# Kernel tuning notes

Hardware: AMD Instinct MI355X
Metric: run time of the kernel (lower is better)

Reference implementation:

```python
import jax, jax.numpy as jnp
import numpy as np

N = 100000
E = 3200000
IN_C, H1, H2 = 512, 64, 32


def gcn_norm(edge_index, edge_weight, num_nodes):
    """PyG gcn_norm with add_self_loops=True: D^-1/2 (A+I) D^-1/2 edge weights."""
    row, col = edge_index[0], edge_index[1]
    loop = jnp.arange(num_nodes, dtype=edge_index.dtype)
    row = jnp.concatenate([row, loop])
    col = jnp.concatenate([col, loop])
    w = jnp.concatenate([edge_weight, jnp.ones((num_nodes,), edge_weight.dtype)])
    deg = jax.ops.segment_sum(w, col, num_segments=num_nodes)
    dinv = jnp.where(deg > 0, jax.lax.rsqrt(jnp.maximum(deg, 1e-12)), 0.0)
    wnorm = dinv[row] * w * dinv[col]
    return row, col, wnorm


def gcn_conv(x, W, b, row, col, wnorm, num_nodes):
    h = x @ W                                   # [N, out] linear first (out <= in)
    msg = wnorm[:, None] * h[row]               # gather + per-edge scale  [E+N, out]
    out = jax.ops.segment_sum(msg, col, num_segments=num_nodes)
    return out + b


def setup_inputs() -> dict:
    key = jax.random.key(0)
    ks = jax.random.split(key, 9)
    x = jax.random.normal(ks[0], (N, IN_C), dtype=jnp.float32)
    edge_index = jax.random.randint(ks[1], (2, E), 0, N, dtype=jnp.int64)
    edge_weight = jax.random.uniform(ks[2], (E,), dtype=jnp.float32)
    # Glorot-style init for GCN linear weights, zero bias (PyG defaults).
    def glorot(k, fan_in, fan_out):
        s = np.sqrt(6.0 / (fan_in + fan_out)).astype(np.float32)
        return jax.random.uniform(k, (fan_in, fan_out), jnp.float32, -s, s)
    return {
        "x": x,
        "edge_index": edge_index,
        "edge_weight": edge_weight,
        "W1": glorot(ks[3], IN_C, H1), "b1": jnp.zeros((H1,), jnp.float32),
        "W2": glorot(ks[4], H1, H2),  "b2": jnp.zeros((H2,), jnp.float32),
        "W3": glorot(ks[5], H2, 1),   "b3": jnp.zeros((1,), jnp.float32),
    }


def reference(x, edge_index, edge_weight, W1, b1, W2, b2, W3, b3):
    # Inference mode: dropout is identity (training=False).
    row, col, wnorm = gcn_norm(edge_index, edge_weight, N)  # cached=True: shared across layers
    h = jax.nn.relu(gcn_conv(x, W1, b1, row, col, wnorm, N))
    h = jax.nn.relu(gcn_conv(h, W2, b2, row, col, wnorm, N))
    h = gcn_conv(h, W3, b3, row, col, wnorm, N)
    return h.reshape(-1)  # [N]
```

## Files before the change

kernel.cpp:

```cpp
#include <hip/hip_runtime.h>

constexpr int BLK = 256;
constexpr int NBLKBIN = 512;
constexpr int MAXNB   = 1024;

typedef __bf16 bf16x8 __attribute__((ext_vector_type(8)));
typedef float  f32x4  __attribute__((ext_vector_type(4)));

__device__ __forceinline__ float blo(unsigned u) { return __uint_as_float(u << 16); }
__device__ __forceinline__ float bhi(unsigned u) { return __uint_as_float(u & 0xffff0000u); }

__device__ __forceinline__ int detect64(const void* ei) {
    const int* p = (const int*)ei;
    int is64 = 1;
#pragma unroll
    for (int i = 0; i < 16; ++i)
        if (p[2 * i + 1] != 0) is64 = 0;
    return is64;
}

__device__ __forceinline__ int load_idx(const void* ei, size_t pos, int is64) {
    if (is64) return (int)((const long long*)ei)[pos];
    return ((const int*)ei)[pos];
}

__global__ void k_prep(const float* __restrict__ W1, const float* __restrict__ W2,
                       __bf16* __restrict__ Wtf, __bf16* __restrict__ Wtf2,
                       int* __restrict__ bkt_cnt, int nb) {
    const int b = blockIdx.x;
    const int t = threadIdx.x;
    if (b < 16) {
        int i = b * 256 + t;
        int lane = i & 63;
        int tt   = (i >> 6) & 3;
        int k0c  = i >> 8;
        int col  = tt * 16 + (lane & 15);
        int kbase = k0c * 32 + (lane >> 4) * 8;
        bf16x8 v;
#pragma unroll
        for (int j = 0; j < 8; ++j) v[j] = (__bf16)W1[(size_t)(kbase + j) * 64 + col];
        *(bf16x8*)(Wtf + (size_t)i * 8) = v;
    } else if (b == 16) {
        int i = t;
        int lane = i & 63;
        int ct   = i >> 6;
        int tt = ct & 1, chunk = ct >> 1;
        int col  = tt * 16 + (lane & 15);
        int kbase = chunk * 32 + (lane >> 4) * 8;
        bf16x8 v;
#pragma unroll
        for (int j = 0; j < 8; ++j) v[j] = (__bf16)W2[(size_t)(kbase + j) * 32 + col];
        *(bf16x8*)(Wtf2 + (size_t)i * 8) = v;
    } else {
        for (int i = t; i < nb; i += 256) bkt_cnt[i] = 0;
    }
}

__global__ __launch_bounds__(256) void k_fat(const void* __restrict__ ei, int e,
                                             int* __restrict__ bucket_cnt,
                                             int* __restrict__ blkbase, int nb,
                                             const float* __restrict__ X,
                                             const __bf16* __restrict__ Wtf,
                                             __bf16* __restrict__ H, int nrows) {
    __shared__ int hist[MAXNB];
    const int t = threadIdx.x;
    if (blockIdx.x < NBLKBIN) {
        for (int b = t; b < nb; b += 256) hist[b] = 0;
        __syncthreads();
        const int is64 = detect64(ei);
        const int chunk = (e + NBLKBIN - 1) / NBLKBIN;
        const int i0 = blockIdx.x * chunk;
        const int i1 = min(e, i0 + chunk);
        for (int i = i0 + t; i < i1; i += 256) {
            int dst = load_idx(ei, (size_t)e + i, is64);
            atomicAdd(&hist[dst >> 7], 1);
        }
        __syncthreads();
        int* myb = blkbase + (size_t)blockIdx.x * MAXNB;
        for (int b = t; b < nb; b += 256) {
            int c = hist[b];
            int base = 0;
            if (c) base = atomicAdd(&bucket_cnt[b], c);
            myb[b] = base;
        }
        return;
    }
    const int bid  = blockIdx.x - NBLKBIN;
    const int wave = t >> 6;
    const int lane = t & 63;
    const int l15  = lane & 15;
    const int lq   = lane >> 4;
    const long rbase = (long)bid * 256 + wave * 64;

    const float4* xr[4];
#pragma unroll
    for (int rg = 0; rg < 4; ++rg) {
        long ar = rbase + rg * 16 + l15;
        if (ar >= nrows) ar = nrows - 1;
        xr[rg] = (const float4*)(X + (size_t)ar * 512) + lq * 2;
    }

    f32x4 acc[4][4];
#pragma unroll
    for (int rg = 0; rg < 4; ++rg)
#pragma unroll
        for (int tt = 0; tt < 4; ++tt) acc[rg][tt] = f32x4{0.f, 0.f, 0.f, 0.f};

    float4 pa[2][4][2];
#pragma unroll
    for (int s = 0; s < 2; ++s)
#pragma unroll
        for (int rg = 0; rg < 4; ++rg) {
            pa[s][rg][0] = xr[rg][s * 8];
            pa[s][rg][1] = xr[rg][s * 8 + 1];
        }

#pragma unroll
    for (int k0c = 0; k0c < 16; ++k0c) {
        const int s = k0c & 1;
        bf16x8 af[4];
#pragma unroll
        for (int rg = 0; rg < 4; ++rg) {
            float4 a0 = pa[s][rg][0], a1 = pa[s][rg][1];
            af[rg][0] = (__bf16)a0.x; af[rg][1] = (__bf16)a0.y;
            af[rg][2] = (__bf16)a0.z; af[rg][3] = (__bf16)a0.w;
            af[rg][4] = (__bf16)a1.x; af[rg][5] = (__bf16)a1.y;
            af[rg][6] = (__bf16)a1.z; af[rg][7] = (__bf16)a1.w;
        }
        if (k0c + 2 < 16) {
#pragma unroll
            for (int rg = 0; rg < 4; ++rg) {
                pa[s][rg][0] = xr[rg][(k0c + 2) * 8];
                pa[s][rg][1] = xr[rg][(k0c + 2) * 8 + 1];
            }
        }
#pragma unroll
        for (int tt = 0; tt < 4; ++tt) {
            bf16x8 bf_ = *(const bf16x8*)(Wtf + ((size_t)(k0c * 4 + tt) * 64 + lane) * 8);
#pragma unroll
            for (int rg = 0; rg < 4; ++rg)
                acc[rg][tt] = __builtin_amdgcn_mfma_f32_16x16x32_bf16(af[rg], bf_, acc[rg][tt], 0, 0, 0);
        }
    }
#pragma unroll
    for (int rg = 0; rg < 4; ++rg)
#pragma unroll
    for (int tt = 0; tt < 4; ++tt)
#pragma unroll
    for (int r = 0; r < 4; ++r) {
        long row = rbase + rg * 16 + lq * 4 + r;
        if (row < nrows) H[(size_t)row * 64 + tt * 16 + l15] = (__bf16)acc[rg][tt][r];
    }
}

__global__ __launch_bounds__(256) void k_binscatter(const void* __restrict__ ei,
                                                    const float* __restrict__ ew, int e,
                                                    const int* __restrict__ bkt_cnt,
                                                    const int* __restrict__ blkbase,
                                                    int2* __restrict__ binned, int nb) {
    __shared__ int scn[256];
    __shared__ int hist[MAXNB];
    const int t = threadIdx.x;
    const int base = t * 4;
    int v[4]; int s = 0;
#pragma unroll
    for (int k = 0; k < 4; ++k) {
        int i = base + k;
        v[k] = (i < nb) ? bkt_cnt[i] : 0;
        s += v[k];
    }
    scn[t] = s;
    __syncthreads();
    for (int d = 1; d < 256; d <<= 1) {
        int x = (t >= d) ? scn[t - d] : 0;
        __syncthreads();
        scn[t] += x;
        __syncthreads();
    }
    int excl = (t == 0) ? 0 : scn[t - 1];
    const int* myb = blkbase + (size_t)blockIdx.x * MAXNB;
#pragma unroll
    for (int k = 0; k < 4; ++k) {
        int i = base + k;
        if (i < nb) hist[i] = excl + myb[i];
        excl += v[k];
    }
    __syncthreads();
    const int is64 = detect64(ei);
    const int chunk = (e + NBLKBIN - 1) / NBLKBIN;
    const int i0 = blockIdx.x * chunk;
    const int i1 = min(e, i0 + chunk);
    for (int i = i0 + t; i < i1; i += 256) {
        int dst = load_idx(ei, (size_t)e + i, is64);
        int src = load_idx(ei, (size_t)i, is64);
        float w = ew[i];
        int bin = dst >> 7;
        int pos = atomicAdd(&hist[bin], 1);
        binned[pos] = make_int2(src | ((dst & 127) << 20), __float_as_int(w));
    }
}

__device__ __forceinline__ void bucket_prefix(const int* __restrict__ bkt_cnt, int nb,
                                              int* scn, int* pfx) {
    const int t = threadIdx.x;
    const int base = t * 4;
    int v[4]; int s = 0;
#pragma unroll
    for (int k = 0; k < 4; ++k) {
        int i = base + k;
        v[k] = (i < nb) ? bkt_cnt[i] : 0;
        s += v[k];
    }
    scn[t] = s;
    __syncthreads();
    for (int d = 1; d < 256; d <<= 1) {
        int x = (t >= d) ? scn[t - d] : 0;
        __syncthreads();
        scn[t] += x;
        __syncthreads();
    }
    int run = (t == 0) ? 0 : scn[t - 1];
#pragma unroll
    for (int k = 0; k < 4; ++k) {
        run += v[k];
        pfx[base + k] = run;
    }
    __syncthreads();
}

__global__ __launch_bounds__(256) void k_degoffs(const int* __restrict__ bkt_cnt,
                                                 const int2* __restrict__ binned,
                                                 float* __restrict__ dinv,
                                                 int* __restrict__ offs, int n, int e, int nb) {
    __shared__ int                scn[256];
    __shared__ int                pfx[MAXNB];
    __shared__ int                icnt[128];
    __shared__ unsigned long long facc[128];
    __shared__ int                scn2[128];
    const int t = threadIdx.x;
    const int b = blockIdx.x;
    bucket_prefix(bkt_cnt, nb, scn, pfx);
    const int j0 = (b == 0) ? 0 : pfx[b - 1];
    const int j1 = pfx[b];
    if (t < 128) { icnt[t] = 0; facc[t] = 0ull; }
    __syncthreads();
    const float SCALE = 1099511627776.f;
    for (int j = j0 + t; j < j1; j += 256) {
        int2 p = binned[j];
        int dl = ((unsigned)p.x) >> 20;
        atomicAdd(&icnt[dl], 1);
        atomicAdd(&facc[dl], (unsigned long long)(__int_as_float(p.y) * SCALE));
    }
    __syncthreads();
    if (t < 128) {
        int nd = b * 128 + t;
        if (nd < n) dinv[nd] = rsqrtf(fmaf((float)facc[t], 1.f / 1099511627776.f, 1.0f));
        scn2[t] = icnt[t];
    }
    __syncthreads();
    for (int d = 1; d < 128; d <<= 1) {
        int x = 0;
        if (t < 128 && t >= d) x = scn2[t - d];
        __syncthreads();
        if (t < 128) scn2[t] += x;
        __syncthreads();
    }
    if (t < 128) {
        int excl = (t == 0) ? 0 : scn2[t - 1];
        int nd = b * 128 + t;
        if (nd < n) offs[nd] = j0 + excl;
    }
    if (b == 0 && t == 0) offs[n] = e;
}

__global__ __launch_bounds__(256) void k_place(const int* __restrict__ bkt_cnt,
                                               const int2* __restrict__ binned,
                                               const int* __restrict__ offs,
                                               const float* __restrict__ dinv,
                                               int2* __restrict__ csrp, int n, int nb) {
    __shared__ int   scn[256];
    __shared__ int   pfx[MAXNB];
    __shared__ int   cur[128];
    __shared__ float ddst[128];
    const int t = threadIdx.x;
    const int b = blockIdx.x;
    bucket_prefix(bkt_cnt, nb, scn, pfx);
    const int j0 = (b == 0) ? 0 : pfx[b - 1];
    const int j1 = pfx[b];
    if (t < 128) {
        int nd = b * 128 + t;
        cur[t]  = (nd < n) ? offs[nd] : 0;
        ddst[t] = (nd < n) ? dinv[nd] : 0.f;
    }
    __syncthreads();
    for (int j = j0 + t; j < j1; j += 256) {
        int2 p = binned[j];
        int dl  = ((unsigned)p.x) >> 20;
        int src = p.x & 0xFFFFF;
        int pos = atomicAdd(&cur[dl], 1);
        float w2 = __int_as_float(p.y) * dinv[src] * ddst[dl];
        csrp[pos] = make_int2(src, __float_as_int(w2));
    }
}

__global__ __launch_bounds__(256) void k_gemm2_mfma(const __bf16* __restrict__ A,
                                                    const __bf16* __restrict__ Wtf2,
                                                    __bf16* __restrict__ H, int nrows) {
    const int wave = threadIdx.x >> 6;
    const int lane = threadIdx.x & 63;
    const int l15  = lane & 15;
    const int lq   = lane >> 4;
    const long rbase = (long)blockIdx.x * 64 + wave * 16;

    long arow = rbase + l15;
    if (arow >= nrows) arow = nrows - 1;

    f32x4 acc[2] = {{0.f,0.f,0.f,0.f},{0.f,0.f,0.f,0.f}};
#pragma unroll
    for (int c = 0; c < 2; ++c) {
        bf16x8 af = *(const bf16x8*)(A + (size_t)arow * 64 + c * 32 + lq * 8);
#pragma unroll
        for (int t = 0; t < 2; ++t) {
            bf16x8 bf_ = *(const bf16x8*)(Wtf2 + ((size_t)(c * 2 + t) * 64 + lane) * 8);
            acc[t] = __builtin_amdgcn_mfma_f32_16x16x32_bf16(af, bf_, acc[t], 0, 0, 0);
        }
    }
#pragma unroll
    for (int t = 0; t < 2; ++t)
#pragma unroll
    for (int r = 0; r < 4; ++r) {
        long row = rbase + lq * 4 + r;
        if (row < nrows) H[(size_t)row * 32 + t * 16 + l15] = (__bf16)acc[t][r];
    }
}

template <int K, int EPI>
__global__ __launch_bounds__(256) void k_prop_bf(const int* __restrict__ offs,
                                                 const int2* __restrict__ csrp,
                                                 const __bf16* __restrict__ hb,
                                                 const float* __restrict__ dinv,
                                                 const float* __restrict__ bias,
                                                 const float* __restrict__ W3,
                                                 void* __restrict__ outv, int n) {
    constexpr int SUB = K / 4;
    constexpr int NPW = 64 / SUB;
    constexpr int NPB = 4 * NPW;
    const int t    = threadIdx.x;
    const int lane = t & 63;
    const int wave = t >> 6;
    const int chq  = lane & (SUB - 1);
    const int sub  = lane / SUB;
    const long nd  = (long)blockIdx.x * NPB + wave * NPW + sub;
    if (nd >= n) return;

    const unsigned short* h = (const unsigned short*)hb;
    const int j0 = offs[nd], j1 = offs[nd + 1];
    float a0 = 0.f, a1 = 0.f, a2 = 0.f, a3 = 0.f;
    int j = j0;
    for (; j + 3 < j1; j += 4) {
        int2 p0 = csrp[j];
        int2 p1 = csrp[j + 1];
        int2 p2 = csrp[j + 2];
        int2 p3 = csrp[j + 3];
        uint2 u0 = *(const uint2*)(h + (size_t)p0.x * K + 4 * chq);
        uint2 u1 = *(const uint2*)(h + (size_t)p1.x * K + 4 * chq);
        uint2 u2 = *(const uint2*)(h + (size_t)p2.x * K + 4 * chq);
        uint2 u3 = *(const uint2*)(h + (size_t)p3.x * K + 4 * chq);
        float w0 = __int_as_float(p0.y), w1 = __int_as_float(p1.y);
        float w2 = __int_as_float(p2.y), w3 = __int_as_float(p3.y);
        a0 = fmaf(w0, blo(u0.x), a0); a1 = fmaf(w0, bhi(u0.x), a1);
        a2 = fmaf(w0, blo(u0.y), a2); a3 = fmaf(w0, bhi(u0.y), a3);
        a0 = fmaf(w1, blo(u1.x), a0); a1 = fmaf(w1, bhi(u1.x), a1);
        a2 = fmaf(w1, blo(u1.y), a2); a3 = fmaf(w1, bhi(u1.y), a3);
        a0 = fmaf(w2, blo(u2.x), a0); a1 = fmaf(w2, bhi(u2.x), a1);
        a2 = fmaf(w2, blo(u2.y), a2); a3 = fmaf(w2, bhi(u2.y), a3);
        a0 = fmaf(w3, blo(u3.x), a0); a1 = fmaf(w3, bhi(u3.x), a1);
        a2 = fmaf(w3, blo(u3.y), a2); a3 = fmaf(w3, bhi(u3.y), a3);
    }
    for (; j < j1; ++j) {
        int2 p0 = csrp[j];
        uint2 u0 = *(const uint2*)(h + (size_t)p0.x * K + 4 * chq);
        float w0 = __int_as_float(p0.y);
        a0 = fmaf(w0, blo(u0.x), a0); a1 = fmaf(w0, bhi(u0.x), a1);
        a2 = fmaf(w0, blo(u0.y), a2); a3 = fmaf(w0, bhi(u0.y), a3);
    }
    const float di = dinv[nd];
    const float s  = di * di;
    uint2 us = *(const uint2*)(h + (size_t)nd * K + 4 * chq);
    float4 bv = *(const float4*)(bias + 4 * chq);
    float o0 = fmaf(s, blo(us.x), a0 + bv.x);
    float o1 = fmaf(s, bhi(us.x), a1 + bv.y);
    float o2 = fmaf(s, blo(us.y), a2 + bv.z);
    float o3 = fmaf(s, bhi(us.y), a3 + bv.w);
    o0 = fmaxf(o0, 0.f); o1 = fmaxf(o1, 0.f); o2 = fmaxf(o2, 0.f); o3 = fmaxf(o3, 0.f);
    if (EPI == 0) {
        unsigned short s0 = __builtin_bit_cast(unsigned short, (__bf16)o0);
        unsigned short s1 = __builtin_bit_cast(unsigned short, (__bf16)o1);
        unsigned short s2 = __builtin_bit_cast(unsigned short, (__bf16)o2);
        unsigned short s3 = __builtin_bit_cast(unsigned short, (__bf16)o3);
        uint2 pk;
        pk.x = (unsigned)s0 | ((unsigned)s1 << 16);
        pk.y = (unsigned)s2 | ((unsigned)s3 << 16);
        *(uint2*)((unsigned*)outv + (size_t)nd * (K / 2) + 2 * chq) = pk;
    } else {
        float4 wv = *(const float4*)(W3 + 4 * chq);
        float part = o0 * wv.x + o1 * wv.y + o2 * wv.z + o3 * wv.w;
#pragma unroll
        for (int d = SUB / 2; d >= 1; d >>= 1) part += __shfl_xor(part, d, SUB);
        if (chq == 0) ((float*)outv)[nd] = part;
    }
}

__global__ __launch_bounds__(256) void k_prop1(const int* __restrict__ offs,
                                               const int2* __restrict__ csrp,
                                               const float* __restrict__ h,
                                               const float* __restrict__ dinv,
                                               const float* __restrict__ bias,
                                               float* __restrict__ out, int n) {
    long nd = (long)blockIdx.x * BLK + threadIdx.x;
    if (nd >= n) return;
    const int j0 = offs[nd], j1 = offs[nd + 1];
    float acc = 0.f;
    int j = j0;
    for (; j + 3 < j1; j += 4) {
        int2 p0 = csrp[j];
        int2 p1 = csrp[j + 1];
        int2 p2 = csrp[j + 2];
        int2 p3 = csrp[j + 3];
        acc = fmaf(__int_as_float(p0.y), h[p0.x], acc);
        acc = fmaf(__int_as_float(p1.y), h[p1.x], acc);
        acc = fmaf(__int_as_float(p2.y), h[p2.x], acc);
        acc = fmaf(__int_as_float(p3.y), h[p3.x], acc);
    }
    for (; j < j1; ++j) {
        int2 p0 = csrp[j];
        acc = fmaf(__int_as_float(p0.y), h[p0.x], acc);
    }
    const float di = dinv[nd];
    out[nd] = fmaf(di * di, h[nd], acc + bias[0]);
}

extern "C" void kernel_launch(void* const* d_in, const int* in_sizes, int n_in,
                              void* d_out, int out_size, void* d_ws, size_t ws_size,
                              hipStream_t stream) {
    const float* x  = (const float*)d_in[0];
    const void*  ei = d_in[1];
    const float* ew = (const float*)d_in[2];
    const float* W1 = (const float*)d_in[3];
    const float* b1 = (const float*)d_in[4];
    const float* W2 = (const float*)d_in[5];
    const float* b2 = (const float*)d_in[6];
    const float* W3 = (const float*)d_in[7];
    const float* b3 = (const float*)d_in[8];
    float* out = (float*)d_out;

    const int n = in_sizes[0] / 512;
    const int e = in_sizes[2];
    const int nb = (n + 127) >> 7;

    char* ws = (char*)d_ws;
    size_t off = 0;
    auto alloc = [&](size_t bytes) {
        void* p = ws + off;
        off = (off + bytes + 255) & ~(size_t)255;
        return p;
    };
    int2*   binned   = (int2*)  alloc((size_t)e * 8);
    int*    bkt_cnt  = (int*)   alloc((size_t)(MAXNB + 1) * 4);
    int*    blkbase  = (int*)   alloc((size_t)NBLKBIN * MAXNB * 4);
    int*    offs     = (int*)   alloc((size_t)(n + 1) * 4);
    int2*   csrp     = (int2*)  alloc((size_t)e * 8);
    float*  dinv     = (float*) alloc((size_t)n * 4);
    __bf16* hb1      = (__bf16*)alloc((size_t)n * 64 * 2);
    __bf16* pb64     = (__bf16*)alloc((size_t)n * 64 * 2);
    __bf16* hbuf2    = (__bf16*)alloc((size_t)n * 32 * 2);
    float*  h3       = (float*) alloc((size_t)n * 4);
    __bf16* Wtf      = (__bf16*)alloc((size_t)512 * 64 * 2);
    __bf16* Wtf2     = (__bf16*)alloc((size_t)64 * 32 * 2);
    (void)ws_size; (void)n_in; (void)out_size;

    const int gb_n = (n + BLK - 1) / BLK;

    k_prep<<<18, 256, 0, stream>>>(W1, W2, Wtf, Wtf2, bkt_cnt, nb);
    k_fat<<<NBLKBIN + (n + 255) / 256, 256, 0, stream>>>(ei, e, bkt_cnt, blkbase, nb,
                                                         x, Wtf, hb1, n);
    k_binscatter<<<NBLKBIN, 256, 0, stream>>>(ei, ew, e, bkt_cnt, blkbase, binned, nb);
    k_degoffs<<<nb, 256, 0, stream>>>(bkt_cnt, binned, dinv, offs, n, e, nb);
    k_place<<<nb, 256, 0, stream>>>(bkt_cnt, binned, offs, dinv, csrp, n, nb);

    k_prop_bf<64, 0><<<(n + 15) / 16, 256, 0, stream>>>(offs, csrp, hb1, dinv, b1, nullptr, pb64, n);
    k_gemm2_mfma<<<(n + 63) / 64, 256, 0, stream>>>(pb64, Wtf2, hbuf2, n);
    k_prop_bf<32, 1><<<(n + 31) / 32, 256, 0, stream>>>(offs, csrp, hbuf2, dinv, b2, W3, h3, n);
    k_prop1<<<gb_n, BLK, 0, stream>>>(offs, csrp, h3, dinv, b3, out, n);
}
```

Measured before the change: 346.5 us.

## Fold degree normalization into GEMM outputs and merge CSR build kernels

Per-edge weights now keep the raw edge weight. The D^-1/2 scaling is applied once per row on the source side, inside the GEMM epilogues and the layer-3 partial, and once per node on the destination side in the propagation epilogues. This lets the degree/offset kernel and the placement kernel merge into one k_build kernel. It drops a random dinv gather per edge and one full pass over the binned edges. The layer-1 GEMM is split out of the histogram kernel so it can run after dinv is known, which gives up the previous overlap of GEMM with histogramming. Propagation kernels also load 8 bf16 channels per lane instead of 4, and the layer-1 hidden buffer now reuses the binned-edge workspace.

```diff
diff --git a/kernel.cpp b/kernel.cpp
--- a/kernel.cpp
+++ b/kernel.cpp
@@ -56,101 +56,57 @@
     }
 }
 
-__global__ __launch_bounds__(256) void k_fat(const void* __restrict__ ei, int e,
-                                             int* __restrict__ bucket_cnt,
-                                             int* __restrict__ blkbase, int nb,
-                                             const float* __restrict__ X,
-                                             const __bf16* __restrict__ Wtf,
-                                             __bf16* __restrict__ H, int nrows) {
+__global__ __launch_bounds__(256) void k_binhist(const void* __restrict__ ei, int e,
+                                                 int* __restrict__ bucket_cnt,
+                                                 int* __restrict__ blkbase, int nb) {
     __shared__ int hist[MAXNB];
     const int t = threadIdx.x;
-    if (blockIdx.x < NBLKBIN) {
-        for (int b = t; b < nb; b += 256) hist[b] = 0;
+    for (int b = t; b < nb; b += 256) hist[b] = 0;
+    __syncthreads();
+    const int is64 = detect64(ei);
+    const int chunk = (e + NBLKBIN - 1) / NBLKBIN;
+    const int i0 = blockIdx.x * chunk;
+    const int i1 = min(e, i0 + chunk);
+    for (int i = i0 + t; i < i1; i += 256) {
+        int dst = load_idx(ei, (size_t)e + i, is64);
+        atomicAdd(&hist[dst >> 7], 1);
+    }
+    __syncthreads();
+    int* myb = blkbase + (size_t)blockIdx.x * MAXNB;
+    for (int b = t; b < nb; b += 256) {
+        int c = hist[b];
+        int base = 0;
+        if (c) base = atomicAdd(&bucket_cnt[b], c);
+        myb[b] = base;
+    }
+}
+
+__device__ __forceinline__ void bucket_prefix(const int* __restrict__ bkt_cnt, int nb,
+                                              int* scn, int* pfx) {
+    const int t = threadIdx.x;
+    const int base = t * 4;
+    int v[4]; int s = 0;
+#pragma unroll
+    for (int k = 0; k < 4; ++k) {
+        int i = base + k;
+        v[k] = (i < nb) ? bkt_cnt[i] : 0;
+        s += v[k];
+    }
+    scn[t] = s;
+    __syncthreads();
+    for (int d = 1; d < 256; d <<= 1) {
+        int x = (t >= d) ? scn[t - d] : 0;
         __syncthreads();
-        const int is64 = detect64(ei);
-        const int chunk = (e + NBLKBIN - 1) / NBLKBIN;
-        const int i0 = blockIdx.x * chunk;
-        const int i1 = min(e, i0 + chunk);
-        for (int i = i0 + t; i < i1; i += 256) {
-            int dst = load_idx(ei, (size_t)e + i, is64);
-            atomicAdd(&hist[dst >> 7], 1);
-        }
+        scn[t] += x;
         __syncthreads();
-        int* myb = blkbase + (size_t)blockIdx.x * MAXNB;
-        for (int b = t; b < nb; b += 256) {
-            int c = hist[b];
-            int base = 0;
-            if (c) base = atomicAdd(&bucket_cnt[b], c);
-            myb[b] = base;
-        }
-        return;
-    }
-    const int bid  = blockIdx.x - NBLKBIN;
-    const int wave = t >> 6;
-    const int lane = t & 63;
-    const int l15  = lane & 15;
-    const int lq   = lane >> 4;
-    const long rbase = (long)bid * 256 + wave * 64;
-
-    const float4* xr[4];
-#pragma unroll
-    for (int rg = 0; rg < 4; ++rg) {
-        long ar = rbase + rg * 16 + l15;
-        if (ar >= nrows) ar = nrows - 1;
-        xr[rg] = (const float4*)(X + (size_t)ar * 512) + lq * 2;
-    }
-
-    f32x4 acc[4][4];
-#pragma unroll
-    for (int rg = 0; rg < 4; ++rg)
-#pragma unroll
-        for (int tt = 0; tt < 4; ++tt) acc[rg][tt] = f32x4{0.f, 0.f, 0.f, 0.f};
-
-    float4 pa[2][4][2];
-#pragma unroll
-    for (int s = 0; s < 2; ++s)
-#pragma unroll
-        for (int rg = 0; rg < 4; ++rg) {
-            pa[s][rg][0] = xr[rg][s * 8];
-            pa[s][rg][1] = xr[rg][s * 8 + 1];
-        }
-
-#pragma unroll
-    for (int k0c = 0; k0c < 16; ++k0c) {
-        const int s = k0c & 1;
-        bf16x8 af[4];
-#pragma unroll
-        for (int rg = 0; rg < 4; ++rg) {
-            float4 a0 = pa[s][rg][0], a1 = pa[s][rg][1];
-            af[rg][0] = (__bf16)a0.x; af[rg][1] = (__bf16)a0.y;
-            af[rg][2] = (__bf16)a0.z; af[rg][3] = (__bf16)a0.w;
-            af[rg][4] = (__bf16)a1.x; af[rg][5] = (__bf16)a1.y;
-            af[rg][6] = (__bf16)a1.z; af[rg][7] = (__bf16)a1.w;
-        }
-        if (k0c + 2 < 16) {
-#pragma unroll
-            for (int rg = 0; rg < 4; ++rg) {
-                pa[s][rg][0] = xr[rg][(k0c + 2) * 8];
-                pa[s][rg][1] = xr[rg][(k0c + 2) * 8 + 1];
-            }
-        }
-#pragma unroll
-        for (int tt = 0; tt < 4; ++tt) {
-            bf16x8 bf_ = *(const bf16x8*)(Wtf + ((size_t)(k0c * 4 + tt) * 64 + lane) * 8);
-#pragma unroll
-            for (int rg = 0; rg < 4; ++rg)
-                acc[rg][tt] = __builtin_amdgcn_mfma_f32_16x16x32_bf16(af[rg], bf_, acc[rg][tt], 0, 0, 0);
-        }
-    }
-#pragma unroll
-    for (int rg = 0; rg < 4; ++rg)
-#pragma unroll
-    for (int tt = 0; tt < 4; ++tt)
-#pragma unroll
-    for (int r = 0; r < 4; ++r) {
-        long row = rbase + rg * 16 + lq * 4 + r;
-        if (row < nrows) H[(size_t)row * 64 + tt * 16 + l15] = (__bf16)acc[rg][tt][r];
-    }
+    }
+    int run = (t == 0) ? 0 : scn[t - 1];
+#pragma unroll
+    for (int k = 0; k < 4; ++k) {
+        run += v[k];
+        pfx[base + k] = run;
+    }
+    __syncthreads();
 }
 
 __global__ __launch_bounds__(256) void k_binscatter(const void* __restrict__ ei,
@@ -200,43 +156,17 @@
     }
 }
 
-__device__ __forceinline__ void bucket_prefix(const int* __restrict__ bkt_cnt, int nb,
-                                              int* scn, int* pfx) {
-    const int t = threadIdx.x;
-    const int base = t * 4;
-    int v[4]; int s = 0;
-#pragma unroll
-    for (int k = 0; k < 4; ++k) {
-        int i = base + k;
-        v[k] = (i < nb) ? bkt_cnt[i] : 0;
-        s += v[k];
-    }
-    scn[t] = s;
-    __syncthreads();
-    for (int d = 1; d < 256; d <<= 1) {
-        int x = (t >= d) ? scn[t - d] : 0;
-        __syncthreads();
-        scn[t] += x;
-        __syncthreads();
-    }
-    int run = (t == 0) ? 0 : scn[t - 1];
-#pragma unroll
-    for (int k = 0; k < 4; ++k) {
-        run += v[k];
-        pfx[base + k] = run;
-    }
-    __syncthreads();
-}
-
-__global__ __launch_bounds__(256) void k_degoffs(const int* __restrict__ bkt_cnt,
-                                                 const int2* __restrict__ binned,
-                                                 float* __restrict__ dinv,
-                                                 int* __restrict__ offs, int n, int e, int nb) {
+__global__ __launch_bounds__(256) void k_build(const int* __restrict__ bkt_cnt,
+                                               const int2* __restrict__ binned,
+                                               float* __restrict__ dinv,
+                                               int* __restrict__ offs,
+                                               int2* __restrict__ csrp, int n, int e, int nb) {
     __shared__ int                scn[256];
     __shared__ int                pfx[MAXNB];
     __shared__ int                icnt[128];
     __shared__ unsigned long long facc[128];
     __shared__ int                scn2[128];
+    __shared__ int                cur[128];
     const int t = threadIdx.x;
     const int b = blockIdx.x;
     bucket_prefix(bkt_cnt, nb, scn, pfx);
@@ -267,44 +197,99 @@
     }
     if (t < 128) {
         int excl = (t == 0) ? 0 : scn2[t - 1];
+        int abs0 = j0 + excl;
+        cur[t] = abs0;
         int nd = b * 128 + t;
-        if (nd < n) offs[nd] = j0 + excl;
+        if (nd < n) offs[nd] = abs0;
     }
     if (b == 0 && t == 0) offs[n] = e;
-}
-
-__global__ __launch_bounds__(256) void k_place(const int* __restrict__ bkt_cnt,
-                                               const int2* __restrict__ binned,
-                                               const int* __restrict__ offs,
-                                               const float* __restrict__ dinv,
-                                               int2* __restrict__ csrp, int n, int nb) {
-    __shared__ int   scn[256];
-    __shared__ int   pfx[MAXNB];
-    __shared__ int   cur[128];
-    __shared__ float ddst[128];
-    const int t = threadIdx.x;
-    const int b = blockIdx.x;
-    bucket_prefix(bkt_cnt, nb, scn, pfx);
-    const int j0 = (b == 0) ? 0 : pfx[b - 1];
-    const int j1 = pfx[b];
-    if (t < 128) {
-        int nd = b * 128 + t;
-        cur[t]  = (nd < n) ? offs[nd] : 0;
-        ddst[t] = (nd < n) ? dinv[nd] : 0.f;
-    }
     __syncthreads();
     for (int j = j0 + t; j < j1; j += 256) {
         int2 p = binned[j];
         int dl  = ((unsigned)p.x) >> 20;
         int src = p.x & 0xFFFFF;
         int pos = atomicAdd(&cur[dl], 1);
-        float w2 = __int_as_float(p.y) * dinv[src] * ddst[dl];
-        csrp[pos] = make_int2(src, __float_as_int(w2));
+        csrp[pos] = make_int2(src, p.y);
+    }
+}
+
+__global__ __launch_bounds__(256) void k_gemm1_mfma(const float* __restrict__ X,
+                                                    const __bf16* __restrict__ Wtf,
+                                                    const float* __restrict__ dinv,
+                                                    __bf16* __restrict__ H, int nrows) {
+    const int wave = threadIdx.x >> 6;
+    const int lane = threadIdx.x & 63;
+    const int l15  = lane & 15;
+    const int lq   = lane >> 4;
+    const long rbase = (long)blockIdx.x * 256 + wave * 64;
+
+    const float4* xr[4];
+#pragma unroll
+    for (int rg = 0; rg < 4; ++rg) {
+        long ar = rbase + rg * 16 + l15;
+        if (ar >= nrows) ar = nrows - 1;
+        xr[rg] = (const float4*)(X + (size_t)ar * 512) + lq * 2;
+    }
+
+    f32x4 acc[4][4];
+#pragma unroll
+    for (int rg = 0; rg < 4; ++rg)
+#pragma unroll
+        for (int tt = 0; tt < 4; ++tt) acc[rg][tt] = f32x4{0.f, 0.f, 0.f, 0.f};
+
+    float4 pa[2][4][2];
+#pragma unroll
+    for (int s = 0; s < 2; ++s)
+#pragma unroll
+        for (int rg = 0; rg < 4; ++rg) {
+            pa[s][rg][0] = xr[rg][s * 8];
+            pa[s][rg][1] = xr[rg][s * 8 + 1];
+        }
+
+#pragma unroll
+    for (int k0c = 0; k0c < 16; ++k0c) {
+        const int s = k0c & 1;
+        bf16x8 af[4];
+#pragma unroll
+        for (int rg = 0; rg < 4; ++rg) {
+            float4 a0 = pa[s][rg][0], a1 = pa[s][rg][1];
+            af[rg][0] = (__bf16)a0.x; af[rg][1] = (__bf16)a0.y;
+            af[rg][2] = (__bf16)a0.z; af[rg][3] = (__bf16)a0.w;
+            af[rg][4] = (__bf16)a1.x; af[rg][5] = (__bf16)a1.y;
+            af[rg][6] = (__bf16)a1.z; af[rg][7] = (__bf16)a1.w;
+        }
+        if (k0c + 2 < 16) {
+#pragma unroll
+            for (int rg = 0; rg < 4; ++rg) {
+                pa[s][rg][0] = xr[rg][(k0c + 2) * 8];
+                pa[s][rg][1] = xr[rg][(k0c + 2) * 8 + 1];
+            }
+        }
+#pragma unroll
+        for (int tt = 0; tt < 4; ++tt) {
+            bf16x8 bf_ = *(const bf16x8*)(Wtf + ((size_t)(k0c * 4 + tt) * 64 + lane) * 8);
+#pragma unroll
+            for (int rg = 0; rg < 4; ++rg)
+                acc[rg][tt] = __builtin_amdgcn_mfma_f32_16x16x32_bf16(af[rg], bf_, acc[rg][tt], 0, 0, 0);
+        }
+    }
+#pragma unroll
+    for (int rg = 0; rg < 4; ++rg)
+#pragma unroll
+    for (int r = 0; r < 4; ++r) {
+        long row = rbase + rg * 16 + lq * 4 + r;
+        if (row < nrows) {
+            float dv = dinv[row];
+#pragma unroll
+            for (int tt = 0; tt < 4; ++tt)
+                H[(size_t)row * 64 + tt * 16 + l15] = (__bf16)(acc[rg][tt][r] * dv);
+        }
     }
 }
 
 __global__ __launch_bounds__(256) void k_gemm2_mfma(const __bf16* __restrict__ A,
                                                     const __bf16* __restrict__ Wtf2,
+                                                    const float* __restrict__ dinv,
                                                     __bf16* __restrict__ H, int nrows) {
     const int wave = threadIdx.x >> 6;
     const int lane = threadIdx.x & 63;
@@ -326,11 +311,14 @@
         }
     }
 #pragma unroll
-    for (int t = 0; t < 2; ++t)
-#pragma unroll
     for (int r = 0; r < 4; ++r) {
         long row = rbase + lq * 4 + r;
-        if (row < nrows) H[(size_t)row * 32 + t * 16 + l15] = (__bf16)acc[t][r];
+        if (row < nrows) {
+            float dv = dinv[row];
+#pragma unroll
+            for (int t = 0; t < 2; ++t)
+                H[(size_t)row * 32 + t * 16 + l15] = (__bf16)(acc[t][r] * dv);
+        }
     }
 }
 
@@ -342,13 +330,13 @@
                                                  const float* __restrict__ bias,
                                                  const float* __restrict__ W3,
                                                  void* __restrict__ outv, int n) {
-    constexpr int SUB = K / 4;
+    constexpr int SUB = K / 8;
     constexpr int NPW = 64 / SUB;
     constexpr int NPB = 4 * NPW;
     const int t    = threadIdx.x;
     const int lane = t & 63;
     const int wave = t >> 6;
-    const int chq  = lane & (SUB - 1);
+    const int cho  = lane & (SUB - 1);
     const int sub  = lane / SUB;
     const long nd  = (long)blockIdx.x * NPB + wave * NPW + sub;
     if (nd >= n) return;
@@ -356,58 +344,78 @@
     const unsigned short* h = (const unsigned short*)hb;
     const int j0 = offs[nd], j1 = offs[nd + 1];
     float a0 = 0.f, a1 = 0.f, a2 = 0.f, a3 = 0.f;
+    float a4 = 0.f, a5 = 0.f, a6 = 0.f, a7 = 0.f;
     int j = j0;
     for (; j + 3 < j1; j += 4) {
         int2 p0 = csrp[j];
         int2 p1 = csrp[j + 1];
         int2 p2 = csrp[j + 2];
         int2 p3 = csrp[j + 3];
-        uint2 u0 = *(const uint2*)(h + (size_t)p0.x * K + 4 * chq);
-        uint2 u1 = *(const uint2*)(h + (size_t)p1.x * K + 4 * chq);
-        uint2 u2 = *(const uint2*)(h + (size_t)p2.x * K + 4 * chq);
-        uint2 u3 = *(const uint2*)(h + (size_t)p3.x * K + 4 * chq);
+        uint4 u0 = *(const uint4*)(h + (size_t)p0.x * K + 8 * cho);
+        uint4 u1 = *(const uint4*)(h + (size_t)p1.x * K + 8 * cho);
+        uint4 u2 = *(const uint4*)(h + (size_t)p2.x * K + 8 * cho);
+        uint4 u3 = *(const uint4*)(h + (size_t)p3.x * K + 8 * cho);
         float w0 = __int_as_float(p0.y), w1 = __int_as_float(p1.y);
         float w2 = __int_as_float(p2.y), w3 = __int_as_float(p3.y);
         a0 = fmaf(w0, blo(u0.x), a0); a1 = fmaf(w0, bhi(u0.x), a1);
         a2 = fmaf(w0, blo(u0.y), a2); a3 = fmaf(w0, bhi(u0.y), a3);
+        a4 = fmaf(w0, blo(u0.z), a4); a5 = fmaf(w0, bhi(u0.z), a5);
+        a6 = fmaf(w0, blo(u0.w), a6); a7 = fmaf(w0, bhi(u0.w), a7);
         a0 = fmaf(w1, blo(u1.x), a0); a1 = fmaf(w1, bhi(u1.x), a1);
         a2 = fmaf(w1, blo(u1.y), a2); a3 = fmaf(w1, bhi(u1.y), a3);
+        a4 = fmaf(w1, blo(u1.z), a4); a5 = fmaf(w1, bhi(u1.z), a5);
+        a6 = fmaf(w1, blo(u1.w), a6); a7 = fmaf(w1, bhi(u1.w), a7);
         a0 = fmaf(w2, blo(u2.x), a0); a1 = fmaf(w2, bhi(u2.x), a1);
         a2 = fmaf(w2, blo(u2.y), a2); a3 = fmaf(w2, bhi(u2.y), a3);
+        a4 = fmaf(w2, blo(u2.z), a4); a5 = fmaf(w2, bhi(u2.z), a5);
+        a6 = fmaf(w2, blo(u2.w), a6); a7 = fmaf(w2, bhi(u2.w), a7);
         a0 = fmaf(w3, blo(u3.x), a0); a1 = fmaf(w3, bhi(u3.x), a1);
         a2 = fmaf(w3, blo(u3.y), a2); a3 = fmaf(w3, bhi(u3.y), a3);
+        a4 = fmaf(w3, blo(u3.z), a4); a5 = fmaf(w3, bhi(u3.z), a5);
+        a6 = fmaf(w3, blo(u3.w), a6); a7 = fmaf(w3, bhi(u3.w), a7);
     }
     for (; j < j1; ++j) {
         int2 p0 = csrp[j];
-        uint2 u0 = *(const uint2*)(h + (size_t)p0.x * K + 4 * chq);
+        uint4 u0 = *(const uint4*)(h + (size_t)p0.x * K + 8 * cho);
         float w0 = __int_as_float(p0.y);
         a0 = fmaf(w0, blo(u0.x), a0); a1 = fmaf(w0, bhi(u0.x), a1);
         a2 = fmaf(w0, blo(u0.y), a2); a3 = fmaf(w0, bhi(u0.y), a3);
+        a4 = fmaf(w0, blo(u0.z), a4); a5 = fmaf(w0, bhi(u0.z), a5);
+        a6 = fmaf(w0, blo(u0.w), a6); a7 = fmaf(w0, bhi(u0.w), a7);
     }
     const float di = dinv[nd];
-    const float s  = di * di;
-    uint2 us = *(const uint2*)(h + (size_t)nd * K + 4 * chq);
-    float4 bv = *(const float4*)(bias + 4 * chq);
-    float o0 = fmaf(s, blo(us.x), a0 + bv.x);
-    float o1 = fmaf(s, bhi(us.x), a1 + bv.y);
-    float o2 = fmaf(s, blo(us.y), a2 + bv.z);
-    float o3 = fmaf(s, bhi(us.y), a3 + bv.w);
+    uint4 us = *(const uint4*)(h + (size_t)nd * K + 8 * cho);
+    float4 bv0 = *(const float4*)(bias + 8 * cho);
+    float4 bv1 = *(const float4*)(bias + 8 * cho + 4);
+    float o0 = fmaf(di, a0 + blo(us.x), bv0.x);
+    float o1 = fmaf(di, a1 + bhi(us.x), bv0.y);
+    float o2 = fmaf(di, a2 + blo(us.y), bv0.z);
+    float o3 = fmaf(di, a3 + bhi(us.y), bv0.w);
+    float o4 = fmaf(di, a4 + blo(us.z), bv1.x);
+    float o5 = fmaf(di, a5 + bhi(us.z), bv1.y);
+    float o6 = fmaf(di, a6 + blo(us.w), bv1.z);
+    float o7 = fmaf(di, a7 + bhi(us.w), bv1.w);
     o0 = fmaxf(o0, 0.f); o1 = fmaxf(o1, 0.f); o2 = fmaxf(o2, 0.f); o3 = fmaxf(o3, 0.f);
+    o4 = fmaxf(o4, 0.f); o5 = fmaxf(o5, 0.f); o6 = fmaxf(o6, 0.f); o7 = fmaxf(o7, 0.f);
     if (EPI == 0) {
-        unsigned short s0 = __builtin_bit_cast(unsigned short, (__bf16)o0);
-        unsigned short s1 = __builtin_bit_cast(unsigned short, (__bf16)o1);
-        unsigned short s2 = __builtin_bit_cast(unsigned short, (__bf16)o2);
-        unsigned short s3 = __builtin_bit_cast(unsigned short, (__bf16)o3);
-        uint2 pk;
-        pk.x = (unsigned)s0 | ((unsigned)s1 << 16);
-        pk.y = (unsigned)s2 | ((unsigned)s3 << 16);
-        *(uint2*)((unsigned*)outv + (size_t)nd * (K / 2) + 2 * chq) = pk;
+        uint4 pk;
+        pk.x = (unsigned)__builtin_bit_cast(unsigned short, (__bf16)o0) |
+               ((unsigned)__builtin_bit_cast(unsigned short, (__bf16)o1) << 16);
+        pk.y = (unsigned)__builtin_bit_cast(unsigned short, (__bf16)o2) |
+               ((unsigned)__builtin_bit_cast(unsigned short, (__bf16)o3) << 16);
+        pk.z = (unsigned)__builtin_bit_cast(unsigned short, (__bf16)o4) |
+               ((unsigned)__builtin_bit_cast(unsigned short, (__bf16)o5) << 16);
+        pk.w = (unsigned)__builtin_bit_cast(unsigned short, (__bf16)o6) |
+               ((unsigned)__builtin_bit_cast(unsigned short, (__bf16)o7) << 16);
+        *(uint4*)((unsigned*)outv + (size_t)nd * (K / 2) + 4 * cho) = pk;
     } else {
-        float4 wv = *(const float4*)(W3 + 4 * chq);
-        float part = o0 * wv.x + o1 * wv.y + o2 * wv.z + o3 * wv.w;
+        float4 wv0 = *(const float4*)(W3 + 8 * cho);
+        float4 wv1 = *(const float4*)(W3 + 8 * cho + 4);
+        float part = o0 * wv0.x + o1 * wv0.y + o2 * wv0.z + o3 * wv0.w
+                   + o4 * wv1.x + o5 * wv1.y + o6 * wv1.z + o7 * wv1.w;
 #pragma unroll
         for (int d = SUB / 2; d >= 1; d >>= 1) part += __shfl_xor(part, d, SUB);
-        if (chq == 0) ((float*)outv)[nd] = part;
+        if (cho == 0) ((float*)outv)[nd] = di * part;
     }
 }
 
@@ -437,7 +445,7 @@
         acc = fmaf(__int_as_float(p0.y), h[p0.x], acc);
     }
     const float di = dinv[nd];
-    out[nd] = fmaf(di * di, h[nd], acc + bias[0]);
+    out[nd] = fmaf(di, acc + h[nd], bias[0]);
 }
 
 extern "C" void kernel_launch(void* const* d_in, const int* in_sizes, int n_in,
@@ -466,12 +474,12 @@
         return p;
     };
     int2*   binned   = (int2*)  alloc((size_t)e * 8);
+    __bf16* hbuf1    = (__bf16*)binned;
     int*    bkt_cnt  = (int*)   alloc((size_t)(MAXNB + 1) * 4);
     int*    blkbase  = (int*)   alloc((size_t)NBLKBIN * MAXNB * 4);
     int*    offs     = (int*)   alloc((size_t)(n + 1) * 4);
     int2*   csrp     = (int2*)  alloc((size_t)e * 8);
     float*  dinv     = (float*) alloc((size_t)n * 4);
-    __bf16* hb1      = (__bf16*)alloc((size_t)n * 64 * 2);
     __bf16* pb64     = (__bf16*)alloc((size_t)n * 64 * 2);
     __bf16* hbuf2    = (__bf16*)alloc((size_t)n * 32 * 2);
     float*  h3       = (float*) alloc((size_t)n * 4);
@@ -482,14 +490,15 @@
     const int gb_n = (n + BLK - 1) / BLK;
 
     k_prep<<<18, 256, 0, stream>>>(W1, W2, Wtf, Wtf2, bkt_cnt, nb);
-    k_fat<<<NBLKBIN + (n + 255) / 256, 256, 0, stream>>>(ei, e, bkt_cnt, blkbase, nb,
-                                                         x, Wtf, hb1, n);
+    k_binhist<<<NBLKBIN, 256, 0, stream>>>(ei, e, bkt_cnt, blkbase, nb);
     k_binscatter<<<NBLKBIN, 256, 0, stream>>>(ei, ew, e, bkt_cnt, blkbase, binned, nb);
-    k_degoffs<<<nb, 256, 0, stream>>>(bkt_cnt, binned, dinv, offs, n, e, nb);
-    k_place<<<nb, 256, 0, stream>>>(bkt_cnt, binned, offs, dinv, csrp, n, nb);
-
-    k_prop_bf<64, 0><<<(n + 15) / 16, 256, 0, stream>>>(offs, csrp, hb1, dinv, b1, nullptr, pb64, n);
-    k_gemm2_mfma<<<(n + 63) / 64, 256, 0, stream>>>(pb64, Wtf2, hbuf2, n);
-    k_prop_bf<32, 1><<<(n + 31) / 32, 256, 0, stream>>>(offs, csrp, hbuf2, dinv, b2, W3, h3, n);
+    k_build<<<nb, 256, 0, stream>>>(bkt_cnt, binned, dinv, offs, csrp, n, e, nb);
+
+    k_gemm1_mfma<<<(n + 255) / 256, 256, 0, stream>>>(x, Wtf, dinv, hbuf1, n);
+    k_prop_bf<64, 0><<<(n + 31) / 32, 256, 0, stream>>>(offs, csrp, hbuf1, dinv, b1, nullptr, pb64, n);
+
+    k_gemm2_mfma<<<(n + 63) / 64, 256, 0, stream>>>(pb64, Wtf2, dinv, hbuf2, n);
+    k_prop_bf<32, 1><<<(n + 63) / 64, 256, 0, stream>>>(offs, csrp, hbuf2, dinv, b2, W3, h3, n);
+
     k_prop1<<<gb_n, BLK, 0, stream>>>(offs, csrp, h3, dinv, b3, out, n);
 }
```

Result: faster. 320.7 us (-7.4%).
